# Kernel tuning notes

Hardware: AMD Instinct MI355X
Metric: run time of the kernel (lower is better)

Reference implementation:

```python
import jax, jax.numpy as jnp
import numpy as np

HID = 2048; H = 16; QLR = 1536; KVLR = 512
DN = 128   # qk_nope_head_dim
DR = 64    # qk_rope_head_dim
DV = 128   # v_head_dim
EPS = 1e-6
B, S = 2, 2048


def rmsnorm(x):
    return x * jax.lax.rsqrt(jnp.mean(x * x, axis=-1, keepdims=True) + EPS)


def rope_tables(seq_len):
    inv_freq = 1.0 / (10000.0 ** (jnp.arange(0, DR, 2, dtype=jnp.float32) / DR))  # [DR/2]
    ang = jnp.arange(seq_len, dtype=jnp.float32)[:, None] * inv_freq[None, :]     # [S, DR/2]
    cos = jnp.concatenate([jnp.cos(ang), jnp.cos(ang)], axis=-1)                  # [S, DR]
    sin = jnp.concatenate([jnp.sin(ang), jnp.sin(ang)], axis=-1)
    return cos, sin


def apply_rope(x, cos, sin):
    # x: [B, h, S, DR]; half-split rotation
    half = DR // 2
    rh = jnp.concatenate([-x[..., half:], x[..., :half]], axis=-1)
    return x * cos + rh * sin


def setup_inputs() -> dict:
    key = jax.random.key(0)
    ks = jax.random.split(key, 7)
    w = 0.02
    inp = {
        "X": jax.random.normal(ks[0], (B, S, HID), dtype=jnp.float32),
        "attention_mask": jnp.tril(jnp.ones((S, S), dtype=jnp.int32)),
        "Wq_down": jax.random.normal(ks[1], (HID, QLR), dtype=jnp.float32) * w,
        "bq_down": jnp.zeros((QLR,), dtype=jnp.float32),
        "Wq_up": jax.random.normal(ks[2], (QLR, H * (DN + DR)), dtype=jnp.float32) * w,
        "bq_up": jnp.zeros((H * (DN + DR),), dtype=jnp.float32),
        "Wkv_down": jax.random.normal(ks[3], (HID, DR + KVLR), dtype=jnp.float32) * w,
        "bkv_down": jnp.zeros((DR + KVLR,), dtype=jnp.float32),
        "Wkv_up": jax.random.normal(ks[4], (KVLR, H * (DN + DV)), dtype=jnp.float32) * w,
        "bkv_up": jnp.zeros((H * (DN + DV),), dtype=jnp.float32),
        "Wo": jax.random.normal(ks[5], (H * DV, HID), dtype=jnp.float32) * w,
        "bo": jnp.zeros((HID,), dtype=jnp.float32),
    }
    return inp


def reference(X, attention_mask, Wq_down, bq_down, Wq_up, bq_up,
              Wkv_down, bkv_down, Wkv_up, bkv_up, Wo, bo):
    b, s, _ = X.shape
    # query path: low-rank down -> RMSNorm -> up
    q = rmsnorm(X @ Wq_down + bq_down) @ Wq_up + bq_up            # [B,S,H*(DN+DR)]
    q = q.reshape(b, s, H, DN + DR).transpose(0, 2, 1, 3)          # [B,H,S,DN+DR]
    q_nope, q_rope = q[..., :DN], q[..., DN:]
    # kv path: shared rope key + compressed latent
    ckv = X @ Wkv_down + bkv_down                                  # [B,S,DR+KVLR]
    k_rope = ckv[..., :DR].reshape(b, s, 1, DR).transpose(0, 2, 1, 3)  # [B,1,S,DR]
    kv = rmsnorm(ckv[..., DR:]) @ Wkv_up + bkv_up                  # [B,S,H*(DN+DV)]
    kv = kv.reshape(b, s, H, DN + DV).transpose(0, 2, 1, 3)        # [B,H,S,DN+DV]
    k_nope, value = kv[..., :DN], kv[..., DN:]
    # decoupled RoPE
    cos, sin = rope_tables(s)
    q_rope = apply_rope(q_rope, cos, sin)
    k_rope = apply_rope(k_rope, cos, sin)
    query = jnp.concatenate([q_nope, q_rope], axis=-1)             # [B,H,S,DN+DR]
    key = jnp.concatenate([k_nope, jnp.broadcast_to(k_rope, (b, H, s, DR))], axis=-1)
    # attention (manual matmul -> mask -> softmax -> matmul; dropout p=0)
    scale = 1.0 / np.sqrt(DN + DR)
    scores = jnp.einsum('bhqd,bhkd->bhqk', query, key) * scale     # [B,H,S,S]
    scores = jnp.where(attention_mask[None, None, :, :] == 0, -jnp.inf, scores)
    probs = jax.nn.softmax(scores, axis=-1)
    attn = jnp.einsum('bhqk,bhkd->bhqd', probs, value)             # [B,H,S,DV]
    attn = attn.transpose(0, 2, 1, 3).reshape(b, s, H * DV)
    return attn @ Wo + bo
```

## Files before the change

### kernel.cpp

```cpp
#include <hip/hip_runtime.h>

#define HID 2048
#define NH 16
#define QLR 1536
#define KVLR 512
#define DN 128
#define DR 64
#define DV 128
#define BB 2
#define SS 2048
#define NTOK (BB*SS)
#define QD 3072
#define KVD 4096
#define CKVD 576
#define NQT (SS/64)

typedef __bf16 bf16x8 __attribute__((ext_vector_type(8)));
typedef float f32x4 __attribute__((ext_vector_type(4)));
typedef unsigned short us4v __attribute__((ext_vector_type(4)));

__device__ __forceinline__ unsigned short f2bf(float f){
  unsigned u = __builtin_bit_cast(unsigned, f);
  return (unsigned short)((u + 0x7fffu + ((u>>16)&1u)) >> 16);
}
__device__ __forceinline__ float bf2f(unsigned short h){
  unsigned u = ((unsigned)h)<<16; return __builtin_bit_cast(float, u);
}
__device__ __forceinline__ unsigned cvt_pk_bf16(float a, float b){
  unsigned r;
  asm("v_cvt_pk_bf16_f32 %0, %1, %2" : "=v"(r) : "v"(a), "v"(b));
  return r;
}

#define GLOAD16(g, l) __builtin_amdgcn_global_load_lds( \
    (const __attribute__((address_space(1))) void*)(const void*)(g), \
    (__attribute__((address_space(3))) void*)(void*)(l), 16, 0, 0)

__global__ void cvt_f32_bf16(const float* __restrict__ in, unsigned short* __restrict__ out, int n4){
  int i = blockIdx.x*256 + threadIdx.x;
  if (i < n4){
    float4 v = ((const float4*)in)[i];
    us4v o = { f2bf(v.x), f2bf(v.y), f2bf(v.z), f2bf(v.w) };
    ((us4v*)out)[i] = o;
  }
}

__global__ void wtrans(const float* __restrict__ W, unsigned short* __restrict__ WT,
                       int K, int N){
  __shared__ float t[32][33];
  int n0 = blockIdx.x*32, k0 = blockIdx.y*32;
  int tx = threadIdx.x & 31, ty = threadIdx.x >> 5;
  #pragma unroll
  for (int i = ty; i < 32; i += 8){
    int k = k0 + i, n = n0 + tx;
    t[i][tx] = (n < N) ? W[(size_t)k*N + n] : 0.f;
  }
  __syncthreads();
  #pragma unroll
  for (int i = ty; i < 32; i += 8){
    int n = n0 + i, k = k0 + tx;
    WT[(size_t)n*K + k] = f2bf(t[tx][i]);
  }
}

template<bool OUTF32>
__device__ __forceinline__ void gemm_core(
  unsigned short* As, unsigned short* Bs,
  const unsigned short* __restrict__ A, int lda,
  const unsigned short* __restrict__ BT,
  const float* __restrict__ bias,
  void* __restrict__ Cv, int ldc,
  int N, int K, int bx, int by)
{
  const int tid = threadIdx.x;
  const int wave = tid>>6, lane = tid&63, lq = lane&15, lg = lane>>4;
  const int tm = by*128, tn = bx*128;
  const int wm = (wave>>1)*64, wn = (wave&1)*64;
  f32x4 acc[4][4] = {};
  char* AsB = (char*)As; char* BsB = (char*)Bs;
  const int r8 = tid>>3;
  const int sc = ((tid&7) ^ (r8&7))*8;
  for (int kt = 0; kt < K; kt += 64){
    __syncthreads();
    #pragma unroll
    for (int rd=0; rd<4; rd++){
      GLOAD16(A  + (size_t)(tm + rd*32 + r8)*lda + kt + sc, AsB + rd*4096 + wave*1024);
      GLOAD16(BT + (size_t)(tn + rd*32 + r8)*K   + kt + sc, BsB + rd*4096 + wave*1024);
    }
    asm volatile("s_waitcnt vmcnt(0)" ::: "memory");
    __syncthreads();
    #pragma unroll
    for (int h=0; h<2; h++){
      bf16x8 af[4], bfr[4];
      #pragma unroll
      for (int i=0;i<4;i++) af[i]  = *(const bf16x8*)(AsB + (wm+16*i+lq)*128 + ((((h*4+lg)^(lq&7)))<<4));
      #pragma unroll
      for (int j=0;j<4;j++) bfr[j] = *(const bf16x8*)(BsB + (wn+16*j+lq)*128 + ((((h*4+lg)^(lq&7)))<<4));
      #pragma unroll
      for (int i=0;i<4;i++)
        #pragma unroll
        for (int j=0;j<4;j++)
          acc[i][j] = __builtin_amdgcn_mfma_f32_16x16x32_bf16(af[i], bfr[j], acc[i][j], 0,0,0);
    }
  }
  #pragma unroll
  for (int i=0;i<4;i++){
    #pragma unroll
    for (int j=0;j<4;j++){
      int col = tn + wn + 16*j + lq;
      if (col < N){
        float bv = bias ? bias[col] : 0.f;
        #pragma unroll
        for (int r=0;r<4;r++){
          int row = tm + wm + 16*i + lg*4 + r;
          float v = acc[i][j][r] + bv;
          if (OUTF32) ((float*)Cv)[(size_t)row*ldc + col] = v;
          else ((unsigned short*)Cv)[(size_t)row*ldc + col] = f2bf(v);
        }
      }
    }
  }
}

template<bool OUTF32>
__global__ __launch_bounds__(256) void gemm_bt(
  const unsigned short* __restrict__ A, int lda,
  const unsigned short* __restrict__ BT,
  const float* __restrict__ bias,
  void* __restrict__ Cv, int ldc, int N, int K)
{
  __shared__ unsigned short As[128*64];
  __shared__ unsigned short Bs[128*64];
  gemm_core<OUTF32>(As, Bs, A, lda, BT, bias, Cv, ldc, N, K, blockIdx.x, blockIdx.y);
}

__global__ __launch_bounds__(256) void gemm_bt_dual(
  const unsigned short* __restrict__ A0, int lda0, const unsigned short* __restrict__ BT0,
  const float* __restrict__ b0, void* __restrict__ C0, int ldc0, int N0, int K0,
  const unsigned short* __restrict__ A1, int lda1, const unsigned short* __restrict__ BT1,
  const float* __restrict__ b1, void* __restrict__ C1, int ldc1, int N1, int K1,
  int split)
{
  __shared__ unsigned short As[128*64];
  __shared__ unsigned short Bs[128*64];
  if ((int)blockIdx.x < split)
    gemm_core<false>(As, Bs, A0, lda0, BT0, b0, C0, ldc0, N0, K0, blockIdx.x, blockIdx.y);
  else
    gemm_core<false>(As, Bs, A1, lda1, BT1, b1, C1, ldc1, N1, K1, blockIdx.x - split, blockIdx.y);
}

__global__ void rms_inplace(unsigned short* __restrict__ buf, int rowlen, int off, int D){
  __shared__ float red[4];
  int row = blockIdx.x, tid = threadIdx.x;
  unsigned short* x = buf + (size_t)row*rowlen + off;
  float ss = 0.f;
  for (int i = tid; i < D; i += 256){ float v = bf2f(x[i]); ss += v*v; }
  #pragma unroll
  for (int o=32;o;o>>=1) ss += __shfl_xor(ss, o, 64);
  if ((tid&63)==0) red[tid>>6] = ss;
  __syncthreads();
  float tot = red[0]+red[1]+red[2]+red[3];
  float sc = rsqrtf(tot/(float)D + 1e-6f);
  for (int i = tid; i < D; i += 256) x[i] = f2bf(bf2f(x[i])*sc);
}

__global__ void rope_q_inplace(unsigned short* __restrict__ q){
  int idx = blockIdx.x*256 + threadIdx.x;
  int j = idx & 31;
  int h = (idx >> 5) & 15;
  int t = idx >> 9;
  int s = t & (SS-1);
  unsigned short* base = q + (size_t)t*QD + h*(DN+DR) + DN;
  float xr = bf2f(base[j]), xi = bf2f(base[j+32]);
  float freq = powf(10000.f, -(float)(2*j)/64.f);
  float ang = (float)s * freq;
  float c = cosf(ang), sn = sinf(ang);
  base[j]    = f2bf(xr*c - xi*sn);
  base[j+32] = f2bf(xi*c + xr*sn);
}

__global__ void rope_k(const unsigned short* __restrict__ ckv, unsigned short* __restrict__ kr){
  int idx = blockIdx.x*256 + threadIdx.x;
  int j = idx & 31;
  int t = idx >> 5;
  int s = t & (SS-1);
  const unsigned short* src = ckv + (size_t)t*CKVD;
  float xr = bf2f(src[j]), xi = bf2f(src[j+32]);
  float freq = powf(10000.f, -(float)(2*j)/64.f);
  float ang = (float)s * freq;
  float c = cosf(ang), sn = sinf(ang);
  kr[(size_t)t*64 + j]      = f2bf(xr*c - xi*sn);
  kr[(size_t)t*64 + j + 32] = f2bf(xi*c + xr*sn);
}

__global__ void transpose_v(const unsigned short* __restrict__ kv, unsigned short* __restrict__ vT){
  __shared__ unsigned short t[32][33];
  int bh = blockIdx.z, b = bh>>4, h = bh&15;
  int s0 = blockIdx.x*32, d0 = blockIdx.y*32;
  int tx = threadIdx.x & 31, ty = threadIdx.x >> 5;
  #pragma unroll
  for (int i = ty; i < 32; i += 8)
    t[i][tx] = kv[((size_t)(b*SS + s0+i))*KVD + h*(DN+DV) + DN + d0 + tx];
  __syncthreads();
  #pragma unroll
  for (int i = ty; i < 32; i += 8)
    vT[((size_t)(bh*DV + d0+i))*SS + s0 + tx] = t[tx][i];
}

__global__ __launch_bounds__(256) void attn_kernel(
  const unsigned short* __restrict__ q,
  const unsigned short* __restrict__ kv,
  const unsigned short* __restrict__ kr,
  const unsigned short* __restrict__ vT,
  unsigned short* __restrict__ attn)
{
  __shared__ unsigned short Ksn[3][32*128];
  __shared__ unsigned short Ksr[3][32*64];
  __shared__ unsigned short Vs [3][128*32];
  __shared__ unsigned short Ps [4*512];
  const int tid = threadIdx.x, wave = tid>>6, lane = tid&63, lq = lane&15, lg = lane>>4;
  const int lin = blockIdx.x;
  const int bh = (lin&7) + 8*((lin>>3)&3);
  const int pairid = lin >> 5;
  const int b = bh>>4, h = bh&15;
  const float kmul = 1.44269504f * 0.07216878364f;

  const int rK = tid>>4, cK = (tid&15) ^ ((tid>>4)&7);
  const int rR = tid>>3, cR = (tid&7) ^ ((tid>>3)&7);
  const unsigned short* gKn0_base = kv + (size_t)(b*SS + rK)*KVD + h*(DN+DV) + cK*8;
  const unsigned short* gKn1_base = gKn0_base + (size_t)16*KVD;
  const unsigned short* gKr_base  = kr + (size_t)(b*SS + rR)*64 + cR*8;
  const unsigned short* gV0_base  = vT + ((size_t)bh*DV + (tid>>2))*SS + (tid&3)*8;
  const unsigned short* gV1_base  = gV0_base + (size_t)64*SS;

#define STAGE_ATTN(bufi) do {                                                 \
    GLOAD16(pKn0, (char*)Ksn[bufi] +        wave*1024);                       \
    GLOAD16(pKn1, (char*)Ksn[bufi] + 4096 + wave*1024);                       \
    GLOAD16(pKr,  (char*)Ksr[bufi] +        wave*1024);                       \
    GLOAD16(pV0,  (char*)Vs[bufi]  +        wave*1024);                       \
    GLOAD16(pV1,  (char*)Vs[bufi]  + 4096 + wave*1024);                       \
    pKn0 += 32*KVD; pKn1 += 32*KVD; pKr += 32*64; pV0 += 32; pV1 += 32;       \
  } while(0)

  for (int half = 0; half < 2; half++){
    const int qt = half ? (NQT-1 - pairid) : pairid;
    const int qw = qt*64 + wave*16;
    const int myq = qw + lq;
    bf16x8 qf[6];
    {
      const unsigned short* qrow = q + (size_t)(b*SS + qw + lq)*QD + h*(DN+DR);
      #pragma unroll
      for (int ks=0;ks<6;ks++) qf[ks] = *(const bf16x8*)(qrow + ks*32 + lg*8);
    }
    f32x4 oacc[8] = {};
    float m = -1e30f, lsum = 0.f;
    const int nkt = 2*qt + 2;

    const unsigned short* pKn0 = gKn0_base;
    const unsigned short* pKn1 = gKn1_base;
    const unsigned short* pKr  = gKr_base;
    const unsigned short* pV0  = gV0_base;
    const unsigned short* pV1  = gV1_base;

    STAGE_ATTN(0);
    STAGE_ATTN(1);
    asm volatile("s_waitcnt vmcnt(5)" ::: "memory");
    __builtin_amdgcn_s_barrier();
    int cur = 0;
    for (int kt = 0; kt < nkt; kt++){
      const bool more = (kt+2 < nkt);
      if (more){ int nb = cur>=1 ? cur-1 : cur+2; STAGE_ATTN(nb); }
      f32x4 sacc[2] = {};
      __builtin_amdgcn_s_setprio(1);
      #pragma unroll
      for (int jf=0;jf<2;jf++){
        const int rowb = jf*16 + lq;
        #pragma unroll
        for (int ks=0;ks<4;ks++){
          bf16x8 kf = *(const bf16x8*)((char*)Ksn[cur] + rowb*256 + ((((ks*4+lg)^(lq&7)))<<4));
          sacc[jf] = __builtin_amdgcn_mfma_f32_16x16x32_bf16(kf, qf[ks], sacc[jf], 0,0,0);
        }
        #pragma unroll
        for (int ks=0;ks<2;ks++){
          bf16x8 kf = *(const bf16x8*)((char*)Ksr[cur] + rowb*128 + ((((ks*4+lg)^(lq&7)))<<4));
          sacc[jf] = __builtin_amdgcn_mfma_f32_16x16x32_bf16(kf, qf[4+ks], sacc[jf], 0,0,0);
        }
      }
      __builtin_amdgcn_s_setprio(0);
      float sv[2][4]; float pmax = -1e30f;
      if (kt*32 + 31 <= qw){
        #pragma unroll
        for (int jf=0;jf<2;jf++)
          #pragma unroll
          for (int r=0;r<4;r++){ float s = sacc[jf][r]*kmul; sv[jf][r]=s; pmax=fmaxf(pmax,s); }
      } else {
        #pragma unroll
        for (int jf=0;jf<2;jf++)
          #pragma unroll
          for (int r=0;r<4;r++){
            int kpos = kt*32 + jf*16 + lg*4 + r;
            float s = (kpos <= myq) ? sacc[jf][r]*kmul : -1e30f;
            sv[jf][r]=s; pmax=fmaxf(pmax,s);
          }
      }
      pmax = fmaxf(pmax, __shfl_xor(pmax, 16, 64));
      pmax = fmaxf(pmax, __shfl_xor(pmax, 32, 64));
      if (!__all(pmax <= m + 8.f)){
        float mnew = fmaxf(m, pmax);
        float alpha = __builtin_amdgcn_exp2f(m - mnew);
        m = mnew;
        lsum *= alpha;
        #pragma unroll
        for (int df=0;df<8;df++)
          #pragma unroll
          for (int r=0;r<4;r++) oacc[df][r] *= alpha;
      }
      float psum = 0.f;
      #pragma unroll
      for (int jf=0;jf<2;jf++){
        float p0 = __builtin_amdgcn_exp2f(sv[jf][0] - m);
        float p1 = __builtin_amdgcn_exp2f(sv[jf][1] - m);
        float p2 = __builtin_amdgcn_exp2f(sv[jf][2] - m);
        float p3 = __builtin_amdgcn_exp2f(sv[jf][3] - m);
        psum += (p0+p1)+(p2+p3);
        uint2 pk = { cvt_pk_bf16(p0,p1), cvt_pk_bf16(p2,p3) };
        *(uint2*)((char*)Ps + wave*1024 + lq*64 + jf*32 + lg*8) = pk;
      }
      psum += __shfl_xor(psum, 16, 64);
      psum += __shfl_xor(psum, 32, 64);
      lsum += psum;
      bf16x8 pf = *(const bf16x8*)((char*)Ps + wave*1024 + lq*64 + lg*16);
      __builtin_amdgcn_s_setprio(1);
      #pragma unroll
      for (int df=0;df<8;df++){
        bf16x8 vf = *(const bf16x8*)(Vs[cur] + (df*16+lq)*32 + lg*8);
        oacc[df] = __builtin_amdgcn_mfma_f32_16x16x32_bf16(vf, pf, oacc[df], 0,0,0);
      }
      __builtin_amdgcn_s_setprio(0);
      if (more) asm volatile("s_waitcnt vmcnt(5)" ::: "memory");
      else      asm volatile("s_waitcnt vmcnt(0)" ::: "memory");
      __builtin_amdgcn_s_barrier();
      cur = cur==2 ? 0 : cur+1;
    }
    float inv = 1.f / lsum;
    #pragma unroll
    for (int df=0;df<8;df++){
      uint2 o = { cvt_pk_bf16(oacc[df][0]*inv, oacc[df][1]*inv),
                  cvt_pk_bf16(oacc[df][2]*inv, oacc[df][3]*inv) };
      *(uint2*)(attn + (size_t)(b*SS + myq)*2048 + h*DV + df*16 + lg*4) = o;
    }
  }
#undef STAGE_ATTN
}

extern "C" void kernel_launch(void* const* d_in, const int* in_sizes, int n_in,
                              void* d_out, int out_size, void* d_ws, size_t ws_size,
                              hipStream_t stream){
  const float* X    = (const float*)d_in[0];
  const float* Wqd  = (const float*)d_in[2];
  const float* bqd  = (const float*)d_in[3];
  const float* Wqu  = (const float*)d_in[4];
  const float* bqu  = (const float*)d_in[5];
  const float* Wkvd = (const float*)d_in[6];
  const float* bkvd = (const float*)d_in[7];
  const float* Wkvu = (const float*)d_in[8];
  const float* bkvu = (const float*)d_in[9];
  const float* Wo   = (const float*)d_in[10];
  const float* bo   = (const float*)d_in[11];
  float* out = (float*)d_out;

  char* ws = (char*)d_ws;
  unsigned short* Xb    = (unsigned short*)(ws + 0);
  unsigned short* attnb = (unsigned short*)(ws + 0);
  char*           arena = ws + 16777216;
  unsigned short* Wt1 = (unsigned short*)(arena);
  unsigned short* Wt3 = (unsigned short*)(arena + 6291456);
  unsigned short* Wt2 = (unsigned short*)(arena);
  unsigned short* Wt4 = (unsigned short*)(arena + 9437184);
  unsigned short* Wt5 = (unsigned short*)(arena);
  unsigned short* cq   = (unsigned short*)(ws + 31457280);
  unsigned short* qtmp = (unsigned short*)(ws + 44040192);
  unsigned short* ckv  = (unsigned short*)(ws + 69206016);
  unsigned short* kvt  = (unsigned short*)(ws + 73924608);
  unsigned short* kr   = (unsigned short*)(ws + 107479040);
  unsigned short* vT   = (unsigned short*)(ws + 108003328);

  cvt_f32_bf16<<<dim3(NTOK*HID/4/256), 256, 0, stream>>>(X, Xb, NTOK*HID/4);
  wtrans<<<dim3(QLR/32, HID/32), 256, 0, stream>>>(Wqd, Wt1, HID, QLR);
  wtrans<<<dim3(640/32, HID/32), 256, 0, stream>>>(Wkvd, Wt3, HID, CKVD);
  gemm_bt_dual<<<dim3(QLR/128 + 640/128, NTOK/128), 256, 0, stream>>>(
      Xb, HID, Wt1, bqd, cq, QLR, QLR, HID,
      Xb, HID, Wt3, bkvd, ckv, CKVD, CKVD, HID, QLR/128);
  rms_inplace<<<dim3(NTOK), 256, 0, stream>>>(cq, QLR, 0, QLR);
  rms_inplace<<<dim3(NTOK), 256, 0, stream>>>(ckv, CKVD, DR, KVLR);
  rope_k<<<dim3(NTOK*32/256), 256, 0, stream>>>(ckv, kr);
  wtrans<<<dim3(QD/32, QLR/32), 256, 0, stream>>>(Wqu, Wt2, QLR, QD);
  wtrans<<<dim3(KVD/32, KVLR/32), 256, 0, stream>>>(Wkvu, Wt4, KVLR, KVD);
  gemm_bt_dual<<<dim3(QD/128 + KVD/128, NTOK/128), 256, 0, stream>>>(
      cq, QLR, Wt2, bqu, qtmp, QD, QD, QLR,
      ckv + DR, CKVD, Wt4, bkvu, kvt, KVD, KVD, KVLR, QD/128);
  rope_q_inplace<<<dim3(NTOK*NH*32/256), 256, 0, stream>>>(qtmp);
  transpose_v<<<dim3(SS/32, DV/32, 32), 256, 0, stream>>>(kvt, vT);
  attn_kernel<<<dim3(NQT/2 * BB*NH), 256, 0, stream>>>(qtmp, kvt, kr, vT, attnb);
  wtrans<<<dim3(HID/32, HID/32), 256, 0, stream>>>(Wo, Wt5, HID, HID);
  gemm_bt<true><<<dim3(HID/128, NTOK/128), 256, 0, stream>>>(attnb, HID, Wt5, bo, out, HID, HID, HID);
}
```

Measured before the change: 363.8 us.

## Remap GEMM blocks across XCDs, fuse small kernels, one q-tile per attention block

GEMM kernels now remap linear block IDs so that consecutive tiles land on the same XCD, aiming for better L2 reuse. The two RMSNorm launches and rope_k are merged into one kernel, and rope_q and the V transpose into another, which removes launch overhead. The attention kernel drops the paired causal q-tile scheme: it now launches one block per q-tile, heaviest tiles first, and moves from triple to double buffering with a full vmcnt(0) wait each iteration. That uses less LDS and may raise occupancy, but the shallower prefetch can expose more load latency.

```diff
diff --git a/kernel.cpp b/kernel.cpp
--- a/kernel.cpp
+++ b/kernel.cpp
@@ -122,6 +122,13 @@
   }
 }
 
+__device__ __forceinline__ void xcd_remap(int& bx, int& by){
+  int nwg = gridDim.x*gridDim.y;
+  int lin = blockIdx.y*gridDim.x + blockIdx.x;
+  int wg = (lin&7)*(nwg>>3) + (lin>>3);
+  bx = wg % gridDim.x; by = wg / gridDim.x;
+}
+
 template<bool OUTF32>
 __global__ __launch_bounds__(256) void gemm_bt(
   const unsigned short* __restrict__ A, int lda,
@@ -131,7 +138,8 @@
 {
   __shared__ unsigned short As[128*64];
   __shared__ unsigned short Bs[128*64];
-  gemm_core<OUTF32>(As, Bs, A, lda, BT, bias, Cv, ldc, N, K, blockIdx.x, blockIdx.y);
+  int bx, by; xcd_remap(bx, by);
+  gemm_core<OUTF32>(As, Bs, A, lda, BT, bias, Cv, ldc, N, K, bx, by);
 }
 
 __global__ __launch_bounds__(256) void gemm_bt_dual(
@@ -143,16 +151,15 @@
 {
   __shared__ unsigned short As[128*64];
   __shared__ unsigned short Bs[128*64];
-  if ((int)blockIdx.x < split)
-    gemm_core<false>(As, Bs, A0, lda0, BT0, b0, C0, ldc0, N0, K0, blockIdx.x, blockIdx.y);
+  int bx, by; xcd_remap(bx, by);
+  if (bx < split)
+    gemm_core<false>(As, Bs, A0, lda0, BT0, b0, C0, ldc0, N0, K0, bx, by);
   else
-    gemm_core<false>(As, Bs, A1, lda1, BT1, b1, C1, ldc1, N1, K1, blockIdx.x - split, blockIdx.y);
-}
-
-__global__ void rms_inplace(unsigned short* __restrict__ buf, int rowlen, int off, int D){
-  __shared__ float red[4];
-  int row = blockIdx.x, tid = threadIdx.x;
-  unsigned short* x = buf + (size_t)row*rowlen + off;
+    gemm_core<false>(As, Bs, A1, lda1, BT1, b1, C1, ldc1, N1, K1, bx - split, by);
+}
+
+__device__ __forceinline__ void rms_row(unsigned short* x, int D, float* red){
+  int tid = threadIdx.x;
   float ss = 0.f;
   for (int i = tid; i < D; i += 256){ float v = bf2f(x[i]); ss += v*v; }
   #pragma unroll
@@ -164,47 +171,61 @@
   for (int i = tid; i < D; i += 256) x[i] = f2bf(bf2f(x[i])*sc);
 }
 
-__global__ void rope_q_inplace(unsigned short* __restrict__ q){
-  int idx = blockIdx.x*256 + threadIdx.x;
-  int j = idx & 31;
-  int h = (idx >> 5) & 15;
-  int t = idx >> 9;
-  int s = t & (SS-1);
-  unsigned short* base = q + (size_t)t*QD + h*(DN+DR) + DN;
-  float xr = bf2f(base[j]), xi = bf2f(base[j+32]);
-  float freq = powf(10000.f, -(float)(2*j)/64.f);
-  float ang = (float)s * freq;
-  float c = cosf(ang), sn = sinf(ang);
-  base[j]    = f2bf(xr*c - xi*sn);
-  base[j+32] = f2bf(xi*c + xr*sn);
-}
-
-__global__ void rope_k(const unsigned short* __restrict__ ckv, unsigned short* __restrict__ kr){
-  int idx = blockIdx.x*256 + threadIdx.x;
-  int j = idx & 31;
-  int t = idx >> 5;
-  int s = t & (SS-1);
-  const unsigned short* src = ckv + (size_t)t*CKVD;
-  float xr = bf2f(src[j]), xi = bf2f(src[j+32]);
-  float freq = powf(10000.f, -(float)(2*j)/64.f);
-  float ang = (float)s * freq;
-  float c = cosf(ang), sn = sinf(ang);
-  kr[(size_t)t*64 + j]      = f2bf(xr*c - xi*sn);
-  kr[(size_t)t*64 + j + 32] = f2bf(xi*c + xr*sn);
-}
-
-__global__ void transpose_v(const unsigned short* __restrict__ kv, unsigned short* __restrict__ vT){
-  __shared__ unsigned short t[32][33];
-  int bh = blockIdx.z, b = bh>>4, h = bh&15;
-  int s0 = blockIdx.x*32, d0 = blockIdx.y*32;
-  int tx = threadIdx.x & 31, ty = threadIdx.x >> 5;
-  #pragma unroll
-  for (int i = ty; i < 32; i += 8)
-    t[i][tx] = kv[((size_t)(b*SS + s0+i))*KVD + h*(DN+DV) + DN + d0 + tx];
-  __syncthreads();
-  #pragma unroll
-  for (int i = ty; i < 32; i += 8)
-    vT[((size_t)(bh*DV + d0+i))*SS + s0 + tx] = t[tx][i];
+__global__ void norms_fused(unsigned short* __restrict__ cq,
+                            unsigned short* __restrict__ ckv,
+                            unsigned short* __restrict__ kr){
+  __shared__ float red[4];
+  int bid = blockIdx.x;
+  if (bid < NTOK){
+    rms_row(cq + (size_t)bid*QLR, QLR, red);
+  } else if (bid < 2*NTOK){
+    rms_row(ckv + (size_t)(bid-NTOK)*CKVD + DR, KVLR, red);
+  } else {
+    int idx = (bid - 2*NTOK)*256 + threadIdx.x;
+    int j = idx & 31;
+    int t = idx >> 5;
+    int s = t & (SS-1);
+    const unsigned short* src = ckv + (size_t)t*CKVD;
+    float xr = bf2f(src[j]), xi = bf2f(src[j+32]);
+    float freq = powf(10000.f, -(float)(2*j)/64.f);
+    float ang = (float)s * freq;
+    float c = cosf(ang), sn = sinf(ang);
+    kr[(size_t)t*64 + j]      = f2bf(xr*c - xi*sn);
+    kr[(size_t)t*64 + j + 32] = f2bf(xi*c + xr*sn);
+  }
+}
+
+__global__ void ropeq_vt_fused(unsigned short* __restrict__ q,
+                               const unsigned short* __restrict__ kv,
+                               unsigned short* __restrict__ vT){
+  int bid = blockIdx.x;
+  if (bid < NTOK*NH*32/256){
+    int idx = bid*256 + threadIdx.x;
+    int j = idx & 31;
+    int h = (idx >> 5) & 15;
+    int t = idx >> 9;
+    int s = t & (SS-1);
+    unsigned short* base = q + (size_t)t*QD + h*(DN+DR) + DN;
+    float xr = bf2f(base[j]), xi = bf2f(base[j+32]);
+    float freq = powf(10000.f, -(float)(2*j)/64.f);
+    float ang = (float)s * freq;
+    float c = cosf(ang), sn = sinf(ang);
+    base[j]    = f2bf(xr*c - xi*sn);
+    base[j+32] = f2bf(xi*c + xr*sn);
+  } else {
+    __shared__ unsigned short t[32][33];
+    int idx = bid - NTOK*NH*32/256;
+    int s0 = (idx & 63)*32, d0 = ((idx>>6)&3)*32, bh = idx>>8;
+    int b = bh>>4, h = bh&15;
+    int tx = threadIdx.x & 31, ty = threadIdx.x >> 5;
+    #pragma unroll
+    for (int i = ty; i < 32; i += 8)
+      t[i][tx] = kv[((size_t)(b*SS + s0+i))*KVD + h*(DN+DV) + DN + d0 + tx];
+    __syncthreads();
+    #pragma unroll
+    for (int i = ty; i < 32; i += 8)
+      vT[((size_t)(bh*DV + d0+i))*SS + s0 + tx] = t[tx][i];
+  }
 }
 
 __global__ __launch_bounds__(256) void attn_kernel(
@@ -214,24 +235,24 @@
   const unsigned short* __restrict__ vT,
   unsigned short* __restrict__ attn)
 {
-  __shared__ unsigned short Ksn[3][32*128];
-  __shared__ unsigned short Ksr[3][32*64];
-  __shared__ unsigned short Vs [3][128*32];
+  __shared__ unsigned short Ksn[2][32*128];
+  __shared__ unsigned short Ksr[2][32*64];
+  __shared__ unsigned short Vs [2][128*32];
   __shared__ unsigned short Ps [4*512];
   const int tid = threadIdx.x, wave = tid>>6, lane = tid&63, lq = lane&15, lg = lane>>4;
   const int lin = blockIdx.x;
   const int bh = (lin&7) + 8*((lin>>3)&3);
-  const int pairid = lin >> 5;
+  const int qt = NQT-1 - (lin>>5);
   const int b = bh>>4, h = bh&15;
   const float kmul = 1.44269504f * 0.07216878364f;
 
   const int rK = tid>>4, cK = (tid&15) ^ ((tid>>4)&7);
   const int rR = tid>>3, cR = (tid&7) ^ ((tid>>3)&7);
-  const unsigned short* gKn0_base = kv + (size_t)(b*SS + rK)*KVD + h*(DN+DV) + cK*8;
-  const unsigned short* gKn1_base = gKn0_base + (size_t)16*KVD;
-  const unsigned short* gKr_base  = kr + (size_t)(b*SS + rR)*64 + cR*8;
-  const unsigned short* gV0_base  = vT + ((size_t)bh*DV + (tid>>2))*SS + (tid&3)*8;
-  const unsigned short* gV1_base  = gV0_base + (size_t)64*SS;
+  const unsigned short* pKn0 = kv + (size_t)(b*SS + rK)*KVD + h*(DN+DV) + cK*8;
+  const unsigned short* pKn1 = pKn0 + (size_t)16*KVD;
+  const unsigned short* pKr  = kr + (size_t)(b*SS + rR)*64 + cR*8;
+  const unsigned short* pV0  = vT + ((size_t)bh*DV + (tid>>2))*SS + (tid&3)*8;
+  const unsigned short* pV1  = pV0 + (size_t)64*SS;
 
 #define STAGE_ATTN(bufi) do {                                                 \
     GLOAD16(pKn0, (char*)Ksn[bufi] +        wave*1024);                       \
@@ -242,113 +263,101 @@
     pKn0 += 32*KVD; pKn1 += 32*KVD; pKr += 32*64; pV0 += 32; pV1 += 32;       \
   } while(0)
 
-  for (int half = 0; half < 2; half++){
-    const int qt = half ? (NQT-1 - pairid) : pairid;
-    const int qw = qt*64 + wave*16;
-    const int myq = qw + lq;
-    bf16x8 qf[6];
-    {
-      const unsigned short* qrow = q + (size_t)(b*SS + qw + lq)*QD + h*(DN+DR);
-      #pragma unroll
-      for (int ks=0;ks<6;ks++) qf[ks] = *(const bf16x8*)(qrow + ks*32 + lg*8);
-    }
-    f32x4 oacc[8] = {};
-    float m = -1e30f, lsum = 0.f;
-    const int nkt = 2*qt + 2;
-
-    const unsigned short* pKn0 = gKn0_base;
-    const unsigned short* pKn1 = gKn1_base;
-    const unsigned short* pKr  = gKr_base;
-    const unsigned short* pV0  = gV0_base;
-    const unsigned short* pV1  = gV1_base;
-
-    STAGE_ATTN(0);
-    STAGE_ATTN(1);
-    asm volatile("s_waitcnt vmcnt(5)" ::: "memory");
+  const int qw = qt*64 + wave*16;
+  const int myq = qw + lq;
+  bf16x8 qf[6];
+  {
+    const unsigned short* qrow = q + (size_t)(b*SS + qw + lq)*QD + h*(DN+DR);
+    #pragma unroll
+    for (int ks=0;ks<6;ks++) qf[ks] = *(const bf16x8*)(qrow + ks*32 + lg*8);
+  }
+  f32x4 oacc[8] = {};
+  float m = -1e30f, lsum = 0.f;
+  const int nkt = 2*qt + 2;
+
+  STAGE_ATTN(0);
+  asm volatile("s_waitcnt vmcnt(0)" ::: "memory");
+  __builtin_amdgcn_s_barrier();
+  int cur = 0;
+  for (int kt = 0; kt < nkt; kt++){
+    if (kt+1 < nkt) STAGE_ATTN(cur^1);
+    f32x4 sacc[2] = {};
+    __builtin_amdgcn_s_setprio(1);
+    #pragma unroll
+    for (int jf=0;jf<2;jf++){
+      const int rowb = jf*16 + lq;
+      #pragma unroll
+      for (int ks=0;ks<4;ks++){
+        bf16x8 kf = *(const bf16x8*)((char*)Ksn[cur] + rowb*256 + ((((ks*4+lg)^(lq&7)))<<4));
+        sacc[jf] = __builtin_amdgcn_mfma_f32_16x16x32_bf16(kf, qf[ks], sacc[jf], 0,0,0);
+      }
+      #pragma unroll
+      for (int ks=0;ks<2;ks++){
+        bf16x8 kf = *(const bf16x8*)((char*)Ksr[cur] + rowb*128 + ((((ks*4+lg)^(lq&7)))<<4));
+        sacc[jf] = __builtin_amdgcn_mfma_f32_16x16x32_bf16(kf, qf[4+ks], sacc[jf], 0,0,0);
+      }
+    }
+    __builtin_amdgcn_s_setprio(0);
+    float sv[2][4]; float pmax = -1e30f;
+    if (kt*32 + 31 <= qw){
+      #pragma unroll
+      for (int jf=0;jf<2;jf++)
+        #pragma unroll
+        for (int r=0;r<4;r++){ float s = sacc[jf][r]*kmul; sv[jf][r]=s; pmax=fmaxf(pmax,s); }
+    } else {
+      #pragma unroll
+      for (int jf=0;jf<2;jf++)
+        #pragma unroll
+        for (int r=0;r<4;r++){
+          int kpos = kt*32 + jf*16 + lg*4 + r;
+          float s = (kpos <= myq) ? sacc[jf][r]*kmul : -1e30f;
+          sv[jf][r]=s; pmax=fmaxf(pmax,s);
+        }
+    }
+    pmax = fmaxf(pmax, __shfl_xor(pmax, 16, 64));
+    pmax = fmaxf(pmax, __shfl_xor(pmax, 32, 64));
+    if (!__all(pmax <= m + 8.f)){
+      float mnew = fmaxf(m, pmax);
+      float alpha = __builtin_amdgcn_exp2f(m - mnew);
+      m = mnew;
+      lsum *= alpha;
+      #pragma unroll
+      for (int df=0;df<8;df++)
+        #pragma unroll
+        for (int r=0;r<4;r++) oacc[df][r] *= alpha;
+    }
+    float psum = 0.f;
+    #pragma unroll
+    for (int jf=0;jf<2;jf++){
+      float p0 = __builtin_amdgcn_exp2f(sv[jf][0] - m);
+      float p1 = __builtin_amdgcn_exp2f(sv[jf][1] - m);
+      float p2 = __builtin_amdgcn_exp2f(sv[jf][2] - m);
+      float p3 = __builtin_amdgcn_exp2f(sv[jf][3] - m);
+      psum += (p0+p1)+(p2+p3);
+      uint2 pk = { cvt_pk_bf16(p0,p1), cvt_pk_bf16(p2,p3) };
+      *(uint2*)((char*)Ps + wave*1024 + lq*64 + jf*32 + lg*8) = pk;
+    }
+    psum += __shfl_xor(psum, 16, 64);
+    psum += __shfl_xor(psum, 32, 64);
+    lsum += psum;
+    bf16x8 pf = *(const bf16x8*)((char*)Ps + wave*1024 + lq*64 + lg*16);
+    __builtin_amdgcn_s_setprio(1);
+    #pragma unroll
+    for (int df=0;df<8;df++){
+      bf16x8 vf = *(const bf16x8*)(Vs[cur] + (df*16+lq)*32 + lg*8);
+      oacc[df] = __builtin_amdgcn_mfma_f32_16x16x32_bf16(vf, pf, oacc[df], 0,0,0);
+    }
+    __builtin_amdgcn_s_setprio(0);
+    asm volatile("s_waitcnt vmcnt(0)" ::: "memory");
     __builtin_amdgcn_s_barrier();
-    int cur = 0;
-    for (int kt = 0; kt < nkt; kt++){
-      const bool more = (kt+2 < nkt);
-      if (more){ int nb = cur>=1 ? cur-1 : cur+2; STAGE_ATTN(nb); }
-      f32x4 sacc[2] = {};
-      __builtin_amdgcn_s_setprio(1);
-      #pragma unroll
-      for (int jf=0;jf<2;jf++){
-        const int rowb = jf*16 + lq;
-        #pragma unroll
-        for (int ks=0;ks<4;ks++){
-          bf16x8 kf = *(const bf16x8*)((char*)Ksn[cur] + rowb*256 + ((((ks*4+lg)^(lq&7)))<<4));
-          sacc[jf] = __builtin_amdgcn_mfma_f32_16x16x32_bf16(kf, qf[ks], sacc[jf], 0,0,0);
-        }
-        #pragma unroll
-        for (int ks=0;ks<2;ks++){
-          bf16x8 kf = *(const bf16x8*)((char*)Ksr[cur] + rowb*128 + ((((ks*4+lg)^(lq&7)))<<4));
-          sacc[jf] = __builtin_amdgcn_mfma_f32_16x16x32_bf16(kf, qf[4+ks], sacc[jf], 0,0,0);
-        }
-      }
-      __builtin_amdgcn_s_setprio(0);
-      float sv[2][4]; float pmax = -1e30f;
-      if (kt*32 + 31 <= qw){
-        #pragma unroll
-        for (int jf=0;jf<2;jf++)
-          #pragma unroll
-          for (int r=0;r<4;r++){ float s = sacc[jf][r]*kmul; sv[jf][r]=s; pmax=fmaxf(pmax,s); }
-      } else {
-        #pragma unroll
-        for (int jf=0;jf<2;jf++)
-          #pragma unroll
-          for (int r=0;r<4;r++){
-            int kpos = kt*32 + jf*16 + lg*4 + r;
-            float s = (kpos <= myq) ? sacc[jf][r]*kmul : -1e30f;
-            sv[jf][r]=s; pmax=fmaxf(pmax,s);
-          }
-      }
-      pmax = fmaxf(pmax, __shfl_xor(pmax, 16, 64));
-      pmax = fmaxf(pmax, __shfl_xor(pmax, 32, 64));
-      if (!__all(pmax <= m + 8.f)){
-        float mnew = fmaxf(m, pmax);
-        float alpha = __builtin_amdgcn_exp2f(m - mnew);
-        m = mnew;
-        lsum *= alpha;
-        #pragma unroll
-        for (int df=0;df<8;df++)
-          #pragma unroll
-          for (int r=0;r<4;r++) oacc[df][r] *= alpha;
-      }
-      float psum = 0.f;
-      #pragma unroll
-      for (int jf=0;jf<2;jf++){
-        float p0 = __builtin_amdgcn_exp2f(sv[jf][0] - m);
-        float p1 = __builtin_amdgcn_exp2f(sv[jf][1] - m);
-        float p2 = __builtin_amdgcn_exp2f(sv[jf][2] - m);
-        float p3 = __builtin_amdgcn_exp2f(sv[jf][3] - m);
-        psum += (p0+p1)+(p2+p3);
-        uint2 pk = { cvt_pk_bf16(p0,p1), cvt_pk_bf16(p2,p3) };
-        *(uint2*)((char*)Ps + wave*1024 + lq*64 + jf*32 + lg*8) = pk;
-      }
-      psum += __shfl_xor(psum, 16, 64);
-      psum += __shfl_xor(psum, 32, 64);
-      lsum += psum;
-      bf16x8 pf = *(const bf16x8*)((char*)Ps + wave*1024 + lq*64 + lg*16);
-      __builtin_amdgcn_s_setprio(1);
-      #pragma unroll
-      for (int df=0;df<8;df++){
-        bf16x8 vf = *(const bf16x8*)(Vs[cur] + (df*16+lq)*32 + lg*8);
-        oacc[df] = __builtin_amdgcn_mfma_f32_16x16x32_bf16(vf, pf, oacc[df], 0,0,0);
-      }
-      __builtin_amdgcn_s_setprio(0);
-      if (more) asm volatile("s_waitcnt vmcnt(5)" ::: "memory");
-      else      asm volatile("s_waitcnt vmcnt(0)" ::: "memory");
-      __builtin_amdgcn_s_barrier();
-      cur = cur==2 ? 0 : cur+1;
-    }
-    float inv = 1.f / lsum;
-    #pragma unroll
-    for (int df=0;df<8;df++){
-      uint2 o = { cvt_pk_bf16(oacc[df][0]*inv, oacc[df][1]*inv),
-                  cvt_pk_bf16(oacc[df][2]*inv, oacc[df][3]*inv) };
-      *(uint2*)(attn + (size_t)(b*SS + myq)*2048 + h*DV + df*16 + lg*4) = o;
-    }
+    cur ^= 1;
+  }
+  float inv = 1.f / lsum;
+  #pragma unroll
+  for (int df=0;df<8;df++){
+    uint2 o = { cvt_pk_bf16(oacc[df][0]*inv, oacc[df][1]*inv),
+                cvt_pk_bf16(oacc[df][2]*inv, oacc[df][3]*inv) };
+    *(uint2*)(attn + (size_t)(b*SS + myq)*2048 + h*DV + df*16 + lg*4) = o;
   }
 #undef STAGE_ATTN
 }
@@ -391,17 +400,14 @@
   gemm_bt_dual<<<dim3(QLR/128 + 640/128, NTOK/128), 256, 0, stream>>>(
       Xb, HID, Wt1, bqd, cq, QLR, QLR, HID,
       Xb, HID, Wt3, bkvd, ckv, CKVD, CKVD, HID, QLR/128);
-  rms_inplace<<<dim3(NTOK), 256, 0, stream>>>(cq, QLR, 0, QLR);
-  rms_inplace<<<dim3(NTOK), 256, 0, stream>>>(ckv, CKVD, DR, KVLR);
-  rope_k<<<dim3(NTOK*32/256), 256, 0, stream>>>(ckv, kr);
+  norms_fused<<<dim3(2*NTOK + NTOK*32/256), 256, 0, stream>>>(cq, ckv, kr);
   wtrans<<<dim3(QD/32, QLR/32), 256, 0, stream>>>(Wqu, Wt2, QLR, QD);
   wtrans<<<dim3(KVD/32, KVLR/32), 256, 0, stream>>>(Wkvu, Wt4, KVLR, KVD);
   gemm_bt_dual<<<dim3(QD/128 + KVD/128, NTOK/128), 256, 0, stream>>>(
       cq, QLR, Wt2, bqu, qtmp, QD, QD, QLR,
       ckv + DR, CKVD, Wt4, bkvu, kvt, KVD, KVD, KVLR, QD/128);
-  rope_q_inplace<<<dim3(NTOK*NH*32/256), 256, 0, stream>>>(qtmp);
-  transpose_v<<<dim3(SS/32, DV/32, 32), 256, 0, stream>>>(kvt, vT);
-  attn_kernel<<<dim3(NQT/2 * BB*NH), 256, 0, stream>>>(qtmp, kvt, kr, vT, attnb);
+  ropeq_vt_fused<<<dim3(NTOK*NH*32/256 + 8192), 256, 0, stream>>>(qtmp, kvt, vT);
+  attn_kernel<<<dim3(NQT * BB*NH), 256, 0, stream>>>(qtmp, kvt, kr, vT, attnb);
   wtrans<<<dim3(HID/32, HID/32), 256, 0, stream>>>(Wo, Wt5, HID, HID);
   gemm_bt<true><<<dim3(HID/128, NTOK/128), 256, 0, stream>>>(attnb, HID, Wt5, bo, out, HID, HID, HID);
 }
```

After: 360.0 us. About the same (-1.1%).
